# Kernel tuning notes

Measured on AMD Instinct MI355X. Metric: run time of the kernel, lower is better.

## Reference

```python
import jax, jax.numpy as jnp
import numpy as np

B, T = 32, 2048
HID, ACT, SRC, AGE = 512, 64, 2, 16
TRUNK, BINS, PHASES = 256, 20, 7
IN_DIM = HID + ACT + SRC + AGE  # 594


def setup_inputs() -> dict:
    key = jax.random.key(0)
    ks = jax.random.split(key, 16)
    s_in = 1.0 / np.sqrt(IN_DIM)
    s_tr = 1.0 / np.sqrt(TRUNK)
    s_h = 1.0 / np.sqrt(HID)
    return {
        "h_t": jax.random.normal(ks[0], (B, T, HID), jnp.float32),
        "a_t": jax.random.normal(ks[1], (B, T, ACT), jnp.float32),
        "d_t": jax.random.normal(ks[2], (B, T, SRC), jnp.float32),
        "age_embed": jax.random.normal(ks[3], (B, T, AGE), jnp.float32),
        "trunk_w": jax.random.normal(ks[4], (IN_DIM, TRUNK), jnp.float32) * s_in,
        "trunk_b": jax.random.normal(ks[5], (TRUNK,), jnp.float32) * s_in,
        "inst_base_w": jax.random.normal(ks[6], (TRUNK, BINS), jnp.float32) * s_tr,
        "inst_base_b": jax.random.normal(ks[7], (BINS,), jnp.float32) * s_tr,
        "group_base_w": jax.random.normal(ks[8], (TRUNK, BINS), jnp.float32) * s_tr,
        "group_base_b": jax.random.normal(ks[9], (BINS,), jnp.float32) * s_tr,
        "inst_exp_w": jax.random.normal(ks[10], (PHASES, TRUNK, BINS), jnp.float32) * s_tr,
        "inst_exp_b": jax.random.normal(ks[11], (PHASES, BINS), jnp.float32) * s_tr,
        "group_exp_w": jax.random.normal(ks[12], (PHASES, TRUNK, BINS), jnp.float32) * s_tr,
        "group_exp_b": jax.random.normal(ks[13], (PHASES, BINS), jnp.float32) * s_tr,
        "router_w": jax.random.normal(ks[14], (HID, PHASES), jnp.float32) * s_h,
        "router_b": jax.random.normal(ks[15], (PHASES,), jnp.float32) * s_h,
    }


def reference(h_t, a_t, d_t, age_embed,
              trunk_w, trunk_b, inst_base_w, inst_base_b,
              group_base_w, group_base_b, inst_exp_w, inst_exp_b,
              group_exp_w, group_exp_b, router_w, router_b):
    # Shared trunk: Linear(594,256) -> exact GELU
    x = jnp.concatenate([h_t, a_t, d_t, age_embed], axis=-1)  # [B,T,594]
    z = jax.nn.gelu(jnp.einsum('bti,io->bto', x, trunk_w) + trunk_b,
                    approximate=False)  # [B,T,256]

    # Soft phase routing from h_t
    pw = jax.nn.softmax(jnp.einsum('bth,hp->btp', h_t, router_w) + router_b,
                        axis=-1)  # [B,T,7]

    # Base heads
    inst_base = jnp.einsum('btd,dk->btk', z, inst_base_w) + inst_base_b
    group_base = jnp.einsum('btd,dk->btk', z, group_base_w) + group_base_b

    # All 7 experts as one batched GEMM, then weighted reduction over phases
    inst_e = jnp.einsum('btd,pdk->btpk', z, inst_exp_w) + inst_exp_b  # [B,T,7,20]
    group_e = jnp.einsum('btd,pdk->btpk', z, group_exp_w) + group_exp_b
    inst_res = jnp.einsum('btp,btpk->btk', pw, inst_e)
    group_res = jnp.einsum('btp,btpk->btk', pw, group_e)

    return (inst_base + inst_res, group_base + group_res)
```

## Files before the change

### kernel.cpp

```cpp
#include <hip/hip_runtime.h>
#include <math.h>

typedef unsigned int uint;
typedef unsigned short ushort;

using short8 = __attribute__((ext_vector_type(8))) short;
using f32x4  = __attribute__((ext_vector_type(4))) float;

#define BT      65536
#define HID     512
#define IN_DIM  594
#define TRUNK   256
#define BINS    20
#define NCOMBO  320

#define WT_P_SZ (19*16*64*8)
#define RP_SZ   (16*64*8)
#define WA_P_SZ (8*20*64*8)

__device__ inline ushort f2bf(float f) {
    uint u = __float_as_uint(f);
    return (ushort)((u + 0x7fffu + ((u >> 16) & 1u)) >> 16);
}

__global__ __launch_bounds__(64) void pack_all(
    const float* __restrict__ trunk_w, const float* __restrict__ router_w,
    const float* __restrict__ inst_base_w, const float* __restrict__ inst_base_b,
    const float* __restrict__ group_base_w, const float* __restrict__ group_base_b,
    const float* __restrict__ inst_exp_w, const float* __restrict__ inst_exp_b,
    const float* __restrict__ group_exp_w, const float* __restrict__ group_exp_b,
    ushort* __restrict__ WtP, ushort* __restrict__ RP,
    ushort* __restrict__ WaP, float* __restrict__ wbias)
{
    const int b = blockIdx.x, l = threadIdx.x;
    const int lr = l & 15, lg = l >> 4;
    if (b < 304) {
        int kk = b >> 4, n = b & 15;
        int col = n * 16 + lr;
        ushort* dst = WtP + ((size_t)(kk * 16 + n) * 64 + l) * 8;
        #pragma unroll
        for (int j = 0; j < 8; ++j) {
            int k = kk * 32 + lg * 8 + j;
            dst[j] = (k < IN_DIM) ? f2bf(trunk_w[k * TRUNK + col]) : (ushort)0;
        }
    } else if (b < 320) {
        int kk = b - 304;
        ushort* dst = RP + ((size_t)(kk * 64 + l)) * 8;
        #pragma unroll
        for (int j = 0; j < 8; ++j) {
            int k = kk * 32 + lg * 8 + j;
            dst[j] = (lr < 7) ? f2bf(router_w[k * 7 + lr]) : (ushort)0;
        }
    } else if (b < 480) {
        int b2 = b - 320, kk = b2 / 20, n = b2 % 20;
        int combo = n * 16 + lr;
        int h = combo / 160, rem = combo % 160, kb = rem >> 3, p = rem & 7;
        const float* bw = h ? group_base_w : inst_base_w;
        const float* ew = h ? group_exp_w  : inst_exp_w;
        ushort* dst = WaP + ((size_t)(kk * 20 + n) * 64 + l) * 8;
        #pragma unroll
        for (int j = 0; j < 8; ++j) {
            int k = kk * 32 + lg * 8 + j;
            float v = (p == 0) ? bw[k * BINS + kb]
                               : ew[((p - 1) * TRUNK + k) * BINS + kb];
            dst[j] = f2bf(v);
        }
    } else {
        for (int c = l; c < NCOMBO; c += 64) {
            int h = c / 160, rem = c % 160, kb = rem >> 3, p = rem & 7;
            const float* bb = h ? group_base_b : inst_base_b;
            const float* eb = h ? group_exp_b  : inst_exp_b;
            wbias[c] = (p == 0) ? bb[kb] : eb[(p - 1) * BINS + kb];
        }
    }
}

__global__ __launch_bounds__(256, 2) void fused_mfma(
    const float* __restrict__ h_t, const float* __restrict__ a_t,
    const float* __restrict__ d_t, const float* __restrict__ age,
    const float* __restrict__ trunk_b, const float* __restrict__ router_b,
    const ushort* __restrict__ WtP, const ushort* __restrict__ RP,
    const ushort* __restrict__ WaP, const float* __restrict__ wbias,
    float* __restrict__ out)
{
    __shared__ alignas(16) ushort zs[32768];

    const int tid = threadIdx.x;
    const int l = tid & 63, w = tid >> 6;
    const int lr = l & 15, lg = l >> 4;
    const int block0 = blockIdx.x * 128;

    const int srow = tid >> 1;
    const int half = tid & 1;
    const size_t stok = block0 + srow;

    ushort* xs = zs;

    f32x4 acc[8][4];
    f32x4 accr0 = (f32x4){0.f,0.f,0.f,0.f};
    f32x4 accr1 = (f32x4){0.f,0.f,0.f,0.f};
    #pragma unroll
    for (int mm = 0; mm < 8; ++mm)
    #pragma unroll
    for (int nn = 0; nn < 4; ++nn) acc[mm][nn] = (f32x4){0.f,0.f,0.f,0.f};

    auto stage_load = [&](int kk, float4 ld[4]) {
        if (kk < 16) {
            const float4* p = (const float4*)(h_t + stok * HID + kk * 32 + half * 16);
            ld[0]=p[0]; ld[1]=p[1]; ld[2]=p[2]; ld[3]=p[3];
        } else if (kk < 18) {
            const float4* p = (const float4*)(a_t + stok * 64 + (kk - 16) * 32 + half * 16);
            ld[0]=p[0]; ld[1]=p[1]; ld[2]=p[2]; ld[3]=p[3];
        } else {
            float* f = (float*)ld;
            #pragma unroll
            for (int j = 0; j < 16; ++j) {
                int c = 576 + half * 16 + j;
                float v;
                if (c < 578)      v = d_t[stok * 2 + (c - 576)];
                else if (c < 594) v = age[stok * 16 + (c - 578)];
                else              v = 0.f;
                f[j] = v;
            }
        }
    };
    auto stage_write = [&](int buf, float4 ld[4]) {
        const float* f = (const float*)ld;
        short8 v0, v1;
        #pragma unroll
        for (int j = 0; j < 8; ++j) {
            v0[j] = (short)f2bf(f[j]);
            v1[j] = (short)f2bf(f[j + 8]);
        }
        ushort* dst = xs + buf * 4096 + (srow >> 4) * 512 + ((srow & 15) + half * 32) * 8;
        *(short8*)dst = v0;
        *(short8*)(dst + 128) = v1;
    };

    {
        float4 ld[4];
        stage_load(0, ld);
        stage_write(0, ld);
        __syncthreads();
        int cur = 0;
        const int w4 = w * 4;
        #pragma unroll 1
        for (int kk = 0; kk < 19; ++kk) {
            float4 nld[4];
            if (kk < 18) stage_load(kk + 1, nld);

            const ushort* wp = WtP + ((size_t)kk * 16 + w4) * 512;
            short8 bq0 = *(const short8*)(wp + 0 * 512 + l * 8);
            short8 bq1 = *(const short8*)(wp + 1 * 512 + l * 8);
            short8 bq2 = *(const short8*)(wp + 2 * 512 + l * 8);
            short8 bq3 = *(const short8*)(wp + 3 * 512 + l * 8);

            const ushort* xb = xs + cur * 4096;
            short8 a0 = *(const short8*)(xb + 0 * 512 + l * 8);
            short8 a1 = *(const short8*)(xb + 1 * 512 + l * 8);
            short8 a2 = *(const short8*)(xb + 2 * 512 + l * 8);
            short8 a3 = *(const short8*)(xb + 3 * 512 + l * 8);
            short8 a4 = *(const short8*)(xb + 4 * 512 + l * 8);
            short8 a5 = *(const short8*)(xb + 5 * 512 + l * 8);
            short8 a6 = *(const short8*)(xb + 6 * 512 + l * 8);
            short8 a7 = *(const short8*)(xb + 7 * 512 + l * 8);

            if (kk < 16) {
                short8 rb = *(const short8*)(RP + (size_t)kk * 512 + l * 8);
                short8 ar0 = *(const short8*)(xb + (w * 2 + 0) * 512 + l * 8);
                short8 ar1 = *(const short8*)(xb + (w * 2 + 1) * 512 + l * 8);
                accr0 = __builtin_amdgcn_mfma_f32_16x16x32_bf16(ar0, rb, accr0, 0, 0, 0);
                accr1 = __builtin_amdgcn_mfma_f32_16x16x32_bf16(ar1, rb, accr1, 0, 0, 0);
            }

            #define TRUNK_MM(AF) \
                acc[0][0] = __builtin_amdgcn_mfma_f32_16x16x32_bf16(AF, bq0, acc[0][0],0,0,0);
            #undef TRUNK_MM
            #pragma unroll
            for (int nn = 0; nn < 4; ++nn) {
                short8 bq = (nn == 0) ? bq0 : (nn == 1) ? bq1 : (nn == 2) ? bq2 : bq3;
                acc[0][nn] = __builtin_amdgcn_mfma_f32_16x16x32_bf16(a0, bq, acc[0][nn],0,0,0);
                acc[1][nn] = __builtin_amdgcn_mfma_f32_16x16x32_bf16(a1, bq, acc[1][nn],0,0,0);
                acc[2][nn] = __builtin_amdgcn_mfma_f32_16x16x32_bf16(a2, bq, acc[2][nn],0,0,0);
                acc[3][nn] = __builtin_amdgcn_mfma_f32_16x16x32_bf16(a3, bq, acc[3][nn],0,0,0);
                acc[4][nn] = __builtin_amdgcn_mfma_f32_16x16x32_bf16(a4, bq, acc[4][nn],0,0,0);
                acc[5][nn] = __builtin_amdgcn_mfma_f32_16x16x32_bf16(a5, bq, acc[5][nn],0,0,0);
                acc[6][nn] = __builtin_amdgcn_mfma_f32_16x16x32_bf16(a6, bq, acc[6][nn],0,0,0);
                acc[7][nn] = __builtin_amdgcn_mfma_f32_16x16x32_bf16(a7, bq, acc[7][nn],0,0,0);
            }

            if (kk < 18) stage_write(cur ^ 1, nld);
            __syncthreads();
            cur ^= 1;
        }
    }

    float pwv[2][4];
    {
        const float rb_l = (lr < 7) ? router_b[lr] : 0.f;
        #pragma unroll
        for (int m = 0; m < 2; ++m)
        #pragma unroll
        for (int r = 0; r < 4; ++r) {
            float lv = (m == 0) ? accr0[r] : accr1[r];
            float x = (lr < 7) ? (lv + rb_l) : -3.0e38f;
            float mx = x;
            mx = fmaxf(mx, __shfl_xor(mx, 1));
            mx = fmaxf(mx, __shfl_xor(mx, 2));
            mx = fmaxf(mx, __shfl_xor(mx, 4));
            mx = fmaxf(mx, __shfl_xor(mx, 8));
            float e = expf(x - mx);
            float s = e;
            s += __shfl_xor(s, 1);
            s += __shfl_xor(s, 2);
            s += __shfl_xor(s, 4);
            s += __shfl_xor(s, 8);
            pwv[m][r] = e / s;
        }
    }

    {
        char* zb = (char*)zs;
        #pragma unroll
        for (int nn = 0; nn < 4; ++nn) {
            float tb = trunk_b[(w * 4 + nn) * 16 + lr];
            int colbase = (w * 4 + nn) * 16 + lr;
            #pragma unroll
            for (int mm = 0; mm < 8; ++mm)
            #pragma unroll
            for (int r = 0; r < 4; ++r) {
                float v = acc[mm][nn][r] + tb;
                v = 0.5f * v * (1.f + erff(v * 0.70710678118654752f));
                int row  = mm * 16 + lg * 4 + r;
                int slot = (colbase >> 3) ^ (row & 7);
                *(ushort*)(zb + row * 512 + slot * 16 + (colbase & 7) * 2) = f2bf(v);
            }
        }
    }
    __syncthreads();

    const char* zb = (const char*)zs;
    const int p8 = l & 7;
    const int csrc = (l & 48) | (p8 ? (p8 - 1) : 0);
    const int row0 = w * 32 + lr;
    const int row1 = row0 + 16;

    float cw[2][4];
    #pragma unroll
    for (int m = 0; m < 2; ++m)
    #pragma unroll
    for (int r = 0; r < 4; ++r)
        cw[m][r] = __shfl(pwv[m][r], csrc);

    #pragma unroll 1
    for (int hf = 0; hf < 2; ++hf) {
        f32x4 acc2[2][10];
        #pragma unroll
        for (int m = 0; m < 2; ++m)
        #pragma unroll
        for (int n = 0; n < 10; ++n) acc2[m][n] = (f32x4){0.f,0.f,0.f,0.f};
        float wb_[10];
        #pragma unroll
        for (int n = 0; n < 10; ++n) wb_[n] = wbias[(hf * 10 + n) * 16 + lr];

        #pragma unroll
        for (int kk = 0; kk < 8; ++kk) {
            short8 a0 = *(const short8*)(zb + row0 * 512 + (((kk * 4 + lg) ^ (row0 & 7)) << 4));
            short8 a1 = *(const short8*)(zb + row1 * 512 + (((kk * 4 + lg) ^ (row1 & 7)) << 4));
            const ushort* wp = WaP + (size_t)(kk * 20 + hf * 10) * 512;
            #pragma unroll
            for (int n = 0; n < 10; ++n) {
                short8 bq = *(const short8*)(wp + (size_t)n * 512 + l * 8);
                acc2[0][n] = __builtin_amdgcn_mfma_f32_16x16x32_bf16(a0, bq, acc2[0][n],0,0,0);
                acc2[1][n] = __builtin_amdgcn_mfma_f32_16x16x32_bf16(a1, bq, acc2[1][n],0,0,0);
            }
        }

        #pragma unroll
        for (int m = 0; m < 2; ++m)
        #pragma unroll
        for (int n = 0; n < 10; ++n)
        #pragma unroll
        for (int r = 0; r < 4; ++r) {
            float e = acc2[m][n][r] + wb_[n];
            float val = (p8 ? cw[m][r] : 1.0f) * e;
            val += __shfl_xor(val, 1);
            val += __shfl_xor(val, 2);
            val += __shfl_xor(val, 4);
            if (p8 == 0) {
                int combo = (hf * 10 + n) * 16 + lr;
                int h = combo / 160, rem = combo % 160, kb = rem >> 3;
                size_t t = block0 + w * 32 + m * 16 + lg * 4 + r;
                out[(size_t)h * (BT * BINS) + t * BINS + kb] = val;
            }
        }
    }
}

extern "C" void kernel_launch(void* const* d_in, const int* in_sizes, int n_in,
                              void* d_out, int out_size, void* d_ws, size_t ws_size,
                              hipStream_t stream) {
    const float* h_t          = (const float*)d_in[0];
    const float* a_t          = (const float*)d_in[1];
    const float* d_t          = (const float*)d_in[2];
    const float* age_embed    = (const float*)d_in[3];
    const float* trunk_w      = (const float*)d_in[4];
    const float* trunk_b      = (const float*)d_in[5];
    const float* inst_base_w  = (const float*)d_in[6];
    const float* inst_base_b  = (const float*)d_in[7];
    const float* group_base_w = (const float*)d_in[8];
    const float* group_base_b = (const float*)d_in[9];
    const float* inst_exp_w   = (const float*)d_in[10];
    const float* inst_exp_b   = (const float*)d_in[11];
    const float* group_exp_w  = (const float*)d_in[12];
    const float* group_exp_b  = (const float*)d_in[13];
    const float* router_w     = (const float*)d_in[14];
    const float* router_b     = (const float*)d_in[15];

    ushort* WtP   = (ushort*)d_ws;
    ushort* RP    = WtP + WT_P_SZ;
    ushort* WaP   = RP + RP_SZ;
    float*  wbias = (float*)(WaP + WA_P_SZ);

    pack_all<<<481, 64, 0, stream>>>(
        trunk_w, router_w,
        inst_base_w, inst_base_b, group_base_w, group_base_b,
        inst_exp_w, inst_exp_b, group_exp_w, group_exp_b,
        WtP, RP, WaP, wbias);

    fused_mfma<<<BT / 128, 256, 0, stream>>>(
        h_t, a_t, d_t, age_embed, trunk_b, router_b,
        WtP, RP, WaP, wbias, (float*)d_out);
}
```

Before: 92.76 us.

## Halve token tile to 64 rows and repartition head GEMM across waves by columns

Each block now handles 64 tokens instead of 128, which halves shared memory and the trunk accumulator registers, and launch bounds are raised to allow three blocks per CU. The head GEMM is changed from a per-wave row split with two column halves to a per-wave column split (five output tiles per wave) over all 64 rows. The router uses the same A fragments as the trunk instead of loading extra ones. The goal is higher occupancy and twice as many blocks. The cost is that each block reloads the trunk and head weights for fewer tokens.

```diff
diff --git a/kernel.cpp b/kernel.cpp
--- a/kernel.cpp
+++ b/kernel.cpp
@@ -75,7 +75,7 @@
     }
 }
 
-__global__ __launch_bounds__(256, 2) void fused_mfma(
+__global__ __launch_bounds__(256, 3) void fused_mfma(
     const float* __restrict__ h_t, const float* __restrict__ a_t,
     const float* __restrict__ d_t, const float* __restrict__ age,
     const float* __restrict__ trunk_b, const float* __restrict__ router_b,
@@ -83,39 +83,40 @@
     const ushort* __restrict__ WaP, const float* __restrict__ wbias,
     float* __restrict__ out)
 {
-    __shared__ alignas(16) ushort zs[32768];
+    __shared__ alignas(16) ushort zs[16384];
 
     const int tid = threadIdx.x;
     const int l = tid & 63, w = tid >> 6;
     const int lr = l & 15, lg = l >> 4;
-    const int block0 = blockIdx.x * 128;
-
-    const int srow = tid >> 1;
-    const int half = tid & 1;
+    const int block0 = blockIdx.x * 64;
+
+    const int srow = tid >> 2;
+    const int sq   = tid & 3;
     const size_t stok = block0 + srow;
 
     ushort* xs = zs;
 
-    f32x4 acc[8][4];
-    f32x4 accr0 = (f32x4){0.f,0.f,0.f,0.f};
-    f32x4 accr1 = (f32x4){0.f,0.f,0.f,0.f};
+    f32x4 acc[4][4];
+    f32x4 accr[4];
     #pragma unroll
-    for (int mm = 0; mm < 8; ++mm)
-    #pragma unroll
-    for (int nn = 0; nn < 4; ++nn) acc[mm][nn] = (f32x4){0.f,0.f,0.f,0.f};
-
-    auto stage_load = [&](int kk, float4 ld[4]) {
+    for (int mm = 0; mm < 4; ++mm) {
+        accr[mm] = (f32x4){0.f,0.f,0.f,0.f};
+        #pragma unroll
+        for (int nn = 0; nn < 4; ++nn) acc[mm][nn] = (f32x4){0.f,0.f,0.f,0.f};
+    }
+
+    auto stage_load = [&](int kk, float4 ld[2]) {
         if (kk < 16) {
-            const float4* p = (const float4*)(h_t + stok * HID + kk * 32 + half * 16);
-            ld[0]=p[0]; ld[1]=p[1]; ld[2]=p[2]; ld[3]=p[3];
+            const float4* p = (const float4*)(h_t + stok * HID + kk * 32 + sq * 8);
+            ld[0] = p[0]; ld[1] = p[1];
         } else if (kk < 18) {
-            const float4* p = (const float4*)(a_t + stok * 64 + (kk - 16) * 32 + half * 16);
-            ld[0]=p[0]; ld[1]=p[1]; ld[2]=p[2]; ld[3]=p[3];
+            const float4* p = (const float4*)(a_t + stok * 64 + (kk - 16) * 32 + sq * 8);
+            ld[0] = p[0]; ld[1] = p[1];
         } else {
             float* f = (float*)ld;
             #pragma unroll
-            for (int j = 0; j < 16; ++j) {
-                int c = 576 + half * 16 + j;
+            for (int j = 0; j < 8; ++j) {
+                int c = 576 + sq * 8 + j;
                 float v;
                 if (c < 578)      v = d_t[stok * 2 + (c - 576)];
                 else if (c < 594) v = age[stok * 16 + (c - 578)];
@@ -124,69 +125,50 @@
             }
         }
     };
-    auto stage_write = [&](int buf, float4 ld[4]) {
+    auto stage_write = [&](int buf, float4 ld[2]) {
         const float* f = (const float*)ld;
-        short8 v0, v1;
-        #pragma unroll
-        for (int j = 0; j < 8; ++j) {
-            v0[j] = (short)f2bf(f[j]);
-            v1[j] = (short)f2bf(f[j + 8]);
-        }
-        ushort* dst = xs + buf * 4096 + (srow >> 4) * 512 + ((srow & 15) + half * 32) * 8;
-        *(short8*)dst = v0;
-        *(short8*)(dst + 128) = v1;
+        short8 v;
+        #pragma unroll
+        for (int j = 0; j < 8; ++j) v[j] = (short)f2bf(f[j]);
+        *(short8*)(xs + buf * 2048 + ((srow >> 4) * 64 + (srow & 15) + sq * 16) * 8) = v;
     };
 
     {
-        float4 ld[4];
+        float4 ld[2];
         stage_load(0, ld);
         stage_write(0, ld);
         __syncthreads();
         int cur = 0;
-        const int w4 = w * 4;
         #pragma unroll 1
         for (int kk = 0; kk < 19; ++kk) {
-            float4 nld[4];
+            float4 nld[2];
             if (kk < 18) stage_load(kk + 1, nld);
 
-            const ushort* wp = WtP + ((size_t)kk * 16 + w4) * 512;
-            short8 bq0 = *(const short8*)(wp + 0 * 512 + l * 8);
-            short8 bq1 = *(const short8*)(wp + 1 * 512 + l * 8);
-            short8 bq2 = *(const short8*)(wp + 2 * 512 + l * 8);
-            short8 bq3 = *(const short8*)(wp + 3 * 512 + l * 8);
-
-            const ushort* xb = xs + cur * 4096;
-            short8 a0 = *(const short8*)(xb + 0 * 512 + l * 8);
-            short8 a1 = *(const short8*)(xb + 1 * 512 + l * 8);
-            short8 a2 = *(const short8*)(xb + 2 * 512 + l * 8);
-            short8 a3 = *(const short8*)(xb + 3 * 512 + l * 8);
-            short8 a4 = *(const short8*)(xb + 4 * 512 + l * 8);
-            short8 a5 = *(const short8*)(xb + 5 * 512 + l * 8);
-            short8 a6 = *(const short8*)(xb + 6 * 512 + l * 8);
-            short8 a7 = *(const short8*)(xb + 7 * 512 + l * 8);
+            const ushort* xb = xs + cur * 2048;
+            short8 a0 = *(const short8*)(xb + (0 * 64 + l) * 8);
+            short8 a1 = *(const short8*)(xb + (1 * 64 + l) * 8);
+            short8 a2 = *(const short8*)(xb + (2 * 64 + l) * 8);
+            short8 a3 = *(const short8*)(xb + (3 * 64 + l) * 8);
+
+            const ushort* wp = WtP + ((size_t)kk * 16 + w * 4) * 512;
+            short8 bq[4];
+            #pragma unroll
+            for (int nn = 0; nn < 4; ++nn)
+                bq[nn] = *(const short8*)(wp + (size_t)nn * 512 + l * 8);
 
             if (kk < 16) {
                 short8 rb = *(const short8*)(RP + (size_t)kk * 512 + l * 8);
-                short8 ar0 = *(const short8*)(xb + (w * 2 + 0) * 512 + l * 8);
-                short8 ar1 = *(const short8*)(xb + (w * 2 + 1) * 512 + l * 8);
-                accr0 = __builtin_amdgcn_mfma_f32_16x16x32_bf16(ar0, rb, accr0, 0, 0, 0);
-                accr1 = __builtin_amdgcn_mfma_f32_16x16x32_bf16(ar1, rb, accr1, 0, 0, 0);
-            }
-
-            #define TRUNK_MM(AF) \
-                acc[0][0] = __builtin_amdgcn_mfma_f32_16x16x32_bf16(AF, bq0, acc[0][0],0,0,0);
-            #undef TRUNK_MM
+                accr[0] = __builtin_amdgcn_mfma_f32_16x16x32_bf16(a0, rb, accr[0],0,0,0);
+                accr[1] = __builtin_amdgcn_mfma_f32_16x16x32_bf16(a1, rb, accr[1],0,0,0);
+                accr[2] = __builtin_amdgcn_mfma_f32_16x16x32_bf16(a2, rb, accr[2],0,0,0);
+                accr[3] = __builtin_amdgcn_mfma_f32_16x16x32_bf16(a3, rb, accr[3],0,0,0);
+            }
             #pragma unroll
             for (int nn = 0; nn < 4; ++nn) {
-                short8 bq = (nn == 0) ? bq0 : (nn == 1) ? bq1 : (nn == 2) ? bq2 : bq3;
-                acc[0][nn] = __builtin_amdgcn_mfma_f32_16x16x32_bf16(a0, bq, acc[0][nn],0,0,0);
-                acc[1][nn] = __builtin_amdgcn_mfma_f32_16x16x32_bf16(a1, bq, acc[1][nn],0,0,0);
-                acc[2][nn] = __builtin_amdgcn_mfma_f32_16x16x32_bf16(a2, bq, acc[2][nn],0,0,0);
-                acc[3][nn] = __builtin_amdgcn_mfma_f32_16x16x32_bf16(a3, bq, acc[3][nn],0,0,0);
-                acc[4][nn] = __builtin_amdgcn_mfma_f32_16x16x32_bf16(a4, bq, acc[4][nn],0,0,0);
-                acc[5][nn] = __builtin_amdgcn_mfma_f32_16x16x32_bf16(a5, bq, acc[5][nn],0,0,0);
-                acc[6][nn] = __builtin_amdgcn_mfma_f32_16x16x32_bf16(a6, bq, acc[6][nn],0,0,0);
-                acc[7][nn] = __builtin_amdgcn_mfma_f32_16x16x32_bf16(a7, bq, acc[7][nn],0,0,0);
+                acc[0][nn] = __builtin_amdgcn_mfma_f32_16x16x32_bf16(a0, bq[nn], acc[0][nn],0,0,0);
+                acc[1][nn] = __builtin_amdgcn_mfma_f32_16x16x32_bf16(a1, bq[nn], acc[1][nn],0,0,0);
+                acc[2][nn] = __builtin_amdgcn_mfma_f32_16x16x32_bf16(a2, bq[nn], acc[2][nn],0,0,0);
+                acc[3][nn] = __builtin_amdgcn_mfma_f32_16x16x32_bf16(a3, bq[nn], acc[3][nn],0,0,0);
             }
 
             if (kk < 18) stage_write(cur ^ 1, nld);
@@ -195,15 +177,14 @@
         }
     }
 
-    float pwv[2][4];
+    float pwv[4][4];
     {
         const float rb_l = (lr < 7) ? router_b[lr] : 0.f;
         #pragma unroll
-        for (int m = 0; m < 2; ++m)
+        for (int mm = 0; mm < 4; ++mm)
         #pragma unroll
         for (int r = 0; r < 4; ++r) {
-            float lv = (m == 0) ? accr0[r] : accr1[r];
-            float x = (lr < 7) ? (lv + rb_l) : -3.0e38f;
+            float x = (lr < 7) ? (accr[mm][r] + rb_l) : -3.0e38f;
             float mx = x;
             mx = fmaxf(mx, __shfl_xor(mx, 1));
             mx = fmaxf(mx, __shfl_xor(mx, 2));
@@ -215,7 +196,7 @@
             s += __shfl_xor(s, 2);
             s += __shfl_xor(s, 4);
             s += __shfl_xor(s, 8);
-            pwv[m][r] = e / s;
+            pwv[mm][r] = e / s;
         }
     }
 
@@ -223,10 +204,10 @@
         char* zb = (char*)zs;
         #pragma unroll
         for (int nn = 0; nn < 4; ++nn) {
-            float tb = trunk_b[(w * 4 + nn) * 16 + lr];
             int colbase = (w * 4 + nn) * 16 + lr;
-            #pragma unroll
-            for (int mm = 0; mm < 8; ++mm)
+            float tb = trunk_b[colbase];
+            #pragma unroll
+            for (int mm = 0; mm < 4; ++mm)
             #pragma unroll
             for (int r = 0; r < 4; ++r) {
                 float v = acc[mm][nn][r] + tb;
@@ -242,56 +223,58 @@
     const char* zb = (const char*)zs;
     const int p8 = l & 7;
     const int csrc = (l & 48) | (p8 ? (p8 - 1) : 0);
-    const int row0 = w * 32 + lr;
-    const int row1 = row0 + 16;
-
-    float cw[2][4];
+
+    f32x4 acc2[4][5];
     #pragma unroll
-    for (int m = 0; m < 2; ++m)
+    for (int mm = 0; mm < 4; ++mm)
     #pragma unroll
-    for (int r = 0; r < 4; ++r)
-        cw[m][r] = __shfl(pwv[m][r], csrc);
-
-    #pragma unroll 1
-    for (int hf = 0; hf < 2; ++hf) {
-        f32x4 acc2[2][10];
-        #pragma unroll
-        for (int m = 0; m < 2; ++m)
-        #pragma unroll
-        for (int n = 0; n < 10; ++n) acc2[m][n] = (f32x4){0.f,0.f,0.f,0.f};
-        float wb_[10];
-        #pragma unroll
-        for (int n = 0; n < 10; ++n) wb_[n] = wbias[(hf * 10 + n) * 16 + lr];
-
-        #pragma unroll
-        for (int kk = 0; kk < 8; ++kk) {
-            short8 a0 = *(const short8*)(zb + row0 * 512 + (((kk * 4 + lg) ^ (row0 & 7)) << 4));
-            short8 a1 = *(const short8*)(zb + row1 * 512 + (((kk * 4 + lg) ^ (row1 & 7)) << 4));
-            const ushort* wp = WaP + (size_t)(kk * 20 + hf * 10) * 512;
-            #pragma unroll
-            for (int n = 0; n < 10; ++n) {
-                short8 bq = *(const short8*)(wp + (size_t)n * 512 + l * 8);
-                acc2[0][n] = __builtin_amdgcn_mfma_f32_16x16x32_bf16(a0, bq, acc2[0][n],0,0,0);
-                acc2[1][n] = __builtin_amdgcn_mfma_f32_16x16x32_bf16(a1, bq, acc2[1][n],0,0,0);
-            }
-        }
-
-        #pragma unroll
-        for (int m = 0; m < 2; ++m)
-        #pragma unroll
-        for (int n = 0; n < 10; ++n)
-        #pragma unroll
-        for (int r = 0; r < 4; ++r) {
-            float e = acc2[m][n][r] + wb_[n];
-            float val = (p8 ? cw[m][r] : 1.0f) * e;
-            val += __shfl_xor(val, 1);
-            val += __shfl_xor(val, 2);
-            val += __shfl_xor(val, 4);
-            if (p8 == 0) {
-                int combo = (hf * 10 + n) * 16 + lr;
-                int h = combo / 160, rem = combo % 160, kb = rem >> 3;
-                size_t t = block0 + w * 32 + m * 16 + lg * 4 + r;
-                out[(size_t)h * (BT * BINS) + t * BINS + kb] = val;
+    for (int nn = 0; nn < 5; ++nn) acc2[mm][nn] = (f32x4){0.f,0.f,0.f,0.f};
+
+    #pragma unroll
+    for (int kk = 0; kk < 8; ++kk) {
+        short8 a[4];
+        #pragma unroll
+        for (int mm = 0; mm < 4; ++mm) {
+            int row = mm * 16 + lr;
+            a[mm] = *(const short8*)(zb + row * 512 + (((kk * 4 + lg) ^ (row & 7)) << 4));
+        }
+        const ushort* wp = WaP + ((size_t)kk * 20 + w * 5) * 512;
+        #pragma unroll
+        for (int nn = 0; nn < 5; ++nn) {
+            short8 bq = *(const short8*)(wp + (size_t)nn * 512 + l * 8);
+            acc2[0][nn] = __builtin_amdgcn_mfma_f32_16x16x32_bf16(a[0], bq, acc2[0][nn],0,0,0);
+            acc2[1][nn] = __builtin_amdgcn_mfma_f32_16x16x32_bf16(a[1], bq, acc2[1][nn],0,0,0);
+            acc2[2][nn] = __builtin_amdgcn_mfma_f32_16x16x32_bf16(a[2], bq, acc2[2][nn],0,0,0);
+            acc2[3][nn] = __builtin_amdgcn_mfma_f32_16x16x32_bf16(a[3], bq, acc2[3][nn],0,0,0);
+        }
+    }
+
+    {
+        float cw[4][4];
+        #pragma unroll
+        for (int mm = 0; mm < 4; ++mm)
+        #pragma unroll
+        for (int r = 0; r < 4; ++r)
+            cw[mm][r] = __shfl(pwv[mm][r], csrc);
+
+        #pragma unroll
+        for (int nn = 0; nn < 5; ++nn) {
+            int combo = (w * 5 + nn) * 16 + lr;
+            float wb = wbias[combo];
+            #pragma unroll
+            for (int mm = 0; mm < 4; ++mm)
+            #pragma unroll
+            for (int r = 0; r < 4; ++r) {
+                float e = acc2[mm][nn][r] + wb;
+                float val = (p8 ? cw[mm][r] : 1.0f) * e;
+                val += __shfl_xor(val, 1);
+                val += __shfl_xor(val, 2);
+                val += __shfl_xor(val, 4);
+                if (p8 == 0) {
+                    int h = combo / 160, rem = combo % 160, kb = rem >> 3;
+                    size_t t = block0 + mm * 16 + lg * 4 + r;
+                    out[(size_t)h * (BT * BINS) + t * BINS + kb] = val;
+                }
             }
         }
     }
@@ -328,7 +311,7 @@
         inst_exp_w, inst_exp_b, group_exp_w, group_exp_b,
         WtP, RP, WaP, wbias);
 
-    fused_mfma<<<BT / 128, 256, 0, stream>>>(
+    fused_mfma<<<BT / 64, 256, 0, stream>>>(
         h_t, a_t, d_t, age_embed, trunk_b, router_b,
         WtP, RP, WaP, wbias, (float*)d_out);
 }
```

After: 110.9 us. 19.6% more time.

## Triple-buffer trunk input staging with two-deep global prefetch and packed bf16 conversion

Applied to the files above, without the earlier changes.

Changes the trunk GEMM staging from a double-buffered LDS ring with one-step prefetch to a three-slot ring. Global loads are issued two k-chunks ahead, while the bf16 conversion and LDS write trail by one chunk. It also switches the float-to-bf16 conversion to the packed __float22bfloat162_rn intrinsic and replaces __syncthreads with an explicit lgkmcnt wait plus s_barrier. The aim is to hide more global-load latency behind the MFMA work and cut conversion ALU cost, at the price of extra registers for the second in-flight load set, which may lower occupancy.

```diff
diff --git a/kernel.cpp b/kernel.cpp
--- a/kernel.cpp
+++ b/kernel.cpp
@@ -1,4 +1,5 @@
 #include <hip/hip_runtime.h>
+#include <hip/hip_bf16.h>
 #include <math.h>
 
 typedef unsigned int uint;
@@ -21,6 +22,20 @@
 __device__ inline ushort f2bf(float f) {
     uint u = __float_as_uint(f);
     return (ushort)((u + 0x7fffu + ((u >> 16) & 1u)) >> 16);
+}
+
+__device__ inline uint pk2(float lo, float hi) {
+    union { __hip_bfloat162 b; uint u; } cv;
+    cv.b = __float22bfloat162_rn(float2{lo, hi});
+    return cv.u;
+}
+__device__ inline short8 cvt8pk(float4 a, float4 b) {
+    union { uint4 t; short8 s; } cv;
+    cv.t.x = pk2(a.x, a.y);
+    cv.t.y = pk2(a.z, a.w);
+    cv.t.z = pk2(b.x, b.y);
+    cv.t.w = pk2(b.z, b.w);
+    return cv.s;
 }
 
 __global__ __launch_bounds__(64) void pack_all(
@@ -104,15 +119,15 @@
     #pragma unroll
     for (int nn = 0; nn < 4; ++nn) acc[mm][nn] = (f32x4){0.f,0.f,0.f,0.f};
 
-    auto stage_load = [&](int kk, float4 ld[4]) {
+    auto stage_load = [&](int kk, float4* dst) {
         if (kk < 16) {
             const float4* p = (const float4*)(h_t + stok * HID + kk * 32 + half * 16);
-            ld[0]=p[0]; ld[1]=p[1]; ld[2]=p[2]; ld[3]=p[3];
+            dst[0]=p[0]; dst[1]=p[1]; dst[2]=p[2]; dst[3]=p[3];
         } else if (kk < 18) {
             const float4* p = (const float4*)(a_t + stok * 64 + (kk - 16) * 32 + half * 16);
-            ld[0]=p[0]; ld[1]=p[1]; ld[2]=p[2]; ld[3]=p[3];
+            dst[0]=p[0]; dst[1]=p[1]; dst[2]=p[2]; dst[3]=p[3];
         } else {
-            float* f = (float*)ld;
+            float* f = (float*)dst;
             #pragma unroll
             for (int j = 0; j < 16; ++j) {
                 int c = 576 + half * 16 + j;
@@ -124,74 +139,61 @@
             }
         }
     };
-    auto stage_write = [&](int buf, float4 ld[4]) {
-        const float* f = (const float*)ld;
-        short8 v0, v1;
-        #pragma unroll
-        for (int j = 0; j < 8; ++j) {
-            v0[j] = (short)f2bf(f[j]);
-            v1[j] = (short)f2bf(f[j + 8]);
-        }
-        ushort* dst = xs + buf * 4096 + (srow >> 4) * 512 + ((srow & 15) + half * 32) * 8;
+    auto stage_write = [&](int slot, const float4* ld) {
+        short8 v0 = cvt8pk(ld[0], ld[1]);
+        short8 v1 = cvt8pk(ld[2], ld[3]);
+        ushort* dst = xs + slot * 4096
+                      + (srow >> 4) * 512 + ((srow & 15) + half * 32) * 8;
         *(short8*)dst = v0;
         *(short8*)(dst + 128) = v1;
     };
 
+    auto mfma_chunk = [&](const ushort* xb, int kk, bool do_router) {
+        short8 a[8];
+        #pragma unroll
+        for (int mm = 0; mm < 8; ++mm)
+            a[mm] = *(const short8*)(xb + (mm * 64 + l) * 8);
+        if (do_router) {
+            short8 rb  = *(const short8*)(RP + (size_t)kk * 512 + l * 8);
+            short8 ar0 = *(const short8*)(xb + ((2 * w + 0) * 64 + l) * 8);
+            short8 ar1 = *(const short8*)(xb + ((2 * w + 1) * 64 + l) * 8);
+            accr0 = __builtin_amdgcn_mfma_f32_16x16x32_bf16(ar0, rb, accr0, 0, 0, 0);
+            accr1 = __builtin_amdgcn_mfma_f32_16x16x32_bf16(ar1, rb, accr1, 0, 0, 0);
+        }
+        const ushort* wp = WtP + ((size_t)kk * 16 + w * 4) * 512;
+        #pragma unroll
+        for (int nn = 0; nn < 4; ++nn) {
+            short8 bq = *(const short8*)(wp + (size_t)nn * 512 + l * 8);
+            acc[0][nn] = __builtin_amdgcn_mfma_f32_16x16x32_bf16(a[0], bq, acc[0][nn],0,0,0);
+            acc[1][nn] = __builtin_amdgcn_mfma_f32_16x16x32_bf16(a[1], bq, acc[1][nn],0,0,0);
+            acc[2][nn] = __builtin_amdgcn_mfma_f32_16x16x32_bf16(a[2], bq, acc[2][nn],0,0,0);
+            acc[3][nn] = __builtin_amdgcn_mfma_f32_16x16x32_bf16(a[3], bq, acc[3][nn],0,0,0);
+            acc[4][nn] = __builtin_amdgcn_mfma_f32_16x16x32_bf16(a[4], bq, acc[4][nn],0,0,0);
+            acc[5][nn] = __builtin_amdgcn_mfma_f32_16x16x32_bf16(a[5], bq, acc[5][nn],0,0,0);
+            acc[6][nn] = __builtin_amdgcn_mfma_f32_16x16x32_bf16(a[6], bq, acc[6][nn],0,0,0);
+            acc[7][nn] = __builtin_amdgcn_mfma_f32_16x16x32_bf16(a[7], bq, acc[7][nn],0,0,0);
+        }
+    };
+
     {
-        float4 ld[4];
-        stage_load(0, ld);
-        stage_write(0, ld);
-        __syncthreads();
-        int cur = 0;
-        const int w4 = w * 4;
+        float4 rA[4], rB[4];
+        stage_load(0, rA);
+        stage_load(1, rB);
+        stage_write(0, rA);
+        asm volatile("s_waitcnt lgkmcnt(0)" ::: "memory");
+        __builtin_amdgcn_s_barrier();
+
         #pragma unroll 1
         for (int kk = 0; kk < 19; ++kk) {
-            float4 nld[4];
-            if (kk < 18) stage_load(kk + 1, nld);
-
-            const ushort* wp = WtP + ((size_t)kk * 16 + w4) * 512;
-            short8 bq0 = *(const short8*)(wp + 0 * 512 + l * 8);
-            short8 bq1 = *(const short8*)(wp + 1 * 512 + l * 8);
-            short8 bq2 = *(const short8*)(wp + 2 * 512 + l * 8);
-            short8 bq3 = *(const short8*)(wp + 3 * 512 + l * 8);
-
-            const ushort* xb = xs + cur * 4096;
-            short8 a0 = *(const short8*)(xb + 0 * 512 + l * 8);
-            short8 a1 = *(const short8*)(xb + 1 * 512 + l * 8);
-            short8 a2 = *(const short8*)(xb + 2 * 512 + l * 8);
-            short8 a3 = *(const short8*)(xb + 3 * 512 + l * 8);
-            short8 a4 = *(const short8*)(xb + 4 * 512 + l * 8);
-            short8 a5 = *(const short8*)(xb + 5 * 512 + l * 8);
-            short8 a6 = *(const short8*)(xb + 6 * 512 + l * 8);
-            short8 a7 = *(const short8*)(xb + 7 * 512 + l * 8);
-
-            if (kk < 16) {
-                short8 rb = *(const short8*)(RP + (size_t)kk * 512 + l * 8);
-                short8 ar0 = *(const short8*)(xb + (w * 2 + 0) * 512 + l * 8);
-                short8 ar1 = *(const short8*)(xb + (w * 2 + 1) * 512 + l * 8);
-                accr0 = __builtin_amdgcn_mfma_f32_16x16x32_bf16(ar0, rb, accr0, 0, 0, 0);
-                accr1 = __builtin_amdgcn_mfma_f32_16x16x32_bf16(ar1, rb, accr1, 0, 0, 0);
-            }
-
-            #define TRUNK_MM(AF) \
-                acc[0][0] = __builtin_amdgcn_mfma_f32_16x16x32_bf16(AF, bq0, acc[0][0],0,0,0);
-            #undef TRUNK_MM
-            #pragma unroll
-            for (int nn = 0; nn < 4; ++nn) {
-                short8 bq = (nn == 0) ? bq0 : (nn == 1) ? bq1 : (nn == 2) ? bq2 : bq3;
-                acc[0][nn] = __builtin_amdgcn_mfma_f32_16x16x32_bf16(a0, bq, acc[0][nn],0,0,0);
-                acc[1][nn] = __builtin_amdgcn_mfma_f32_16x16x32_bf16(a1, bq, acc[1][nn],0,0,0);
-                acc[2][nn] = __builtin_amdgcn_mfma_f32_16x16x32_bf16(a2, bq, acc[2][nn],0,0,0);
-                acc[3][nn] = __builtin_amdgcn_mfma_f32_16x16x32_bf16(a3, bq, acc[3][nn],0,0,0);
-                acc[4][nn] = __builtin_amdgcn_mfma_f32_16x16x32_bf16(a4, bq, acc[4][nn],0,0,0);
-                acc[5][nn] = __builtin_amdgcn_mfma_f32_16x16x32_bf16(a5, bq, acc[5][nn],0,0,0);
-                acc[6][nn] = __builtin_amdgcn_mfma_f32_16x16x32_bf16(a6, bq, acc[6][nn],0,0,0);
-                acc[7][nn] = __builtin_amdgcn_mfma_f32_16x16x32_bf16(a7, bq, acc[7][nn],0,0,0);
-            }
-
-            if (kk < 18) stage_write(cur ^ 1, nld);
-            __syncthreads();
-            cur ^= 1;
+            float4 rC[4];
+            if (kk + 2 < 19) stage_load(kk + 2, rC);
+            mfma_chunk(xs + (kk % 3) * 4096, kk, kk < 16);
+            if (kk + 1 < 19) stage_write((kk + 1) % 3, rB);
+            asm volatile("s_waitcnt lgkmcnt(0)" ::: "memory");
+            __builtin_amdgcn_s_barrier();
+            if (kk + 2 < 19) {
+                rB[0] = rC[0]; rB[1] = rC[1]; rB[2] = rC[2]; rB[3] = rC[3];
+            }
         }
     }
 
@@ -223,8 +225,8 @@
         char* zb = (char*)zs;
         #pragma unroll
         for (int nn = 0; nn < 4; ++nn) {
-            float tb = trunk_b[(w * 4 + nn) * 16 + lr];
             int colbase = (w * 4 + nn) * 16 + lr;
+            float tb = trunk_b[colbase];
             #pragma unroll
             for (int mm = 0; mm < 8; ++mm)
             #pragma unroll
```

Result: slower. 106.8 us (+15.2%).

## Retile head GEMM as 2x2 wave grid and pack bf16 conversions

Applied to the files above, without the earlier changes.

The second-stage head GEMM changes from each wave owning 32 rows and all 10 column tiles to a 2x2 wave split. Each wave now owns 64 rows and 5 column tiles per half, so every B fragment loaded from global memory feeds 4 MFMAs instead of 2, halving weight traffic per block. Routing weights are exchanged through a small shared-memory table instead of lane shuffles, and the staging conversion to bf16 uses packed float2-to-bfloat162 intrinsics. In exchange there are more LDS A-fragment reads, extra LDS for the routing table, and possibly higher register pressure.

```diff
diff --git a/kernel.cpp b/kernel.cpp
--- a/kernel.cpp
+++ b/kernel.cpp
@@ -1,4 +1,5 @@
 #include <hip/hip_runtime.h>
+#include <hip/hip_bf16.h>
 #include <math.h>
 
 typedef unsigned int uint;
@@ -21,6 +22,20 @@
 __device__ inline ushort f2bf(float f) {
     uint u = __float_as_uint(f);
     return (ushort)((u + 0x7fffu + ((u >> 16) & 1u)) >> 16);
+}
+
+__device__ inline uint pk2(float lo, float hi) {
+    union { __hip_bfloat162 b; uint u; } cv;
+    cv.b = __float22bfloat162_rn(float2{lo, hi});
+    return cv.u;
+}
+__device__ inline short8 cvt8pk(float4 a, float4 b) {
+    union { uint4 t; short8 s; } cv;
+    cv.t.x = pk2(a.x, a.y);
+    cv.t.y = pk2(a.z, a.w);
+    cv.t.z = pk2(b.x, b.y);
+    cv.t.w = pk2(b.z, b.w);
+    return cv.s;
 }
 
 __global__ __launch_bounds__(64) void pack_all(
@@ -84,6 +99,7 @@
     float* __restrict__ out)
 {
     __shared__ alignas(16) ushort zs[32768];
+    __shared__ float pwl[128 * 9];
 
     const int tid = threadIdx.x;
     const int l = tid & 63, w = tid >> 6;
@@ -125,13 +141,8 @@
         }
     };
     auto stage_write = [&](int buf, float4 ld[4]) {
-        const float* f = (const float*)ld;
-        short8 v0, v1;
-        #pragma unroll
-        for (int j = 0; j < 8; ++j) {
-            v0[j] = (short)f2bf(f[j]);
-            v1[j] = (short)f2bf(f[j + 8]);
-        }
+        short8 v0 = cvt8pk(ld[0], ld[1]);
+        short8 v1 = cvt8pk(ld[2], ld[3]);
         ushort* dst = xs + buf * 4096 + (srow >> 4) * 512 + ((srow & 15) + half * 32) * 8;
         *(short8*)dst = v0;
         *(short8*)(dst + 128) = v1;
@@ -173,9 +184,6 @@
                 accr1 = __builtin_amdgcn_mfma_f32_16x16x32_bf16(ar1, rb, accr1, 0, 0, 0);
             }
 
-            #define TRUNK_MM(AF) \
-                acc[0][0] = __builtin_amdgcn_mfma_f32_16x16x32_bf16(AF, bq0, acc[0][0],0,0,0);
-            #undef TRUNK_MM
             #pragma unroll
             for (int nn = 0; nn < 4; ++nn) {
                 short8 bq = (nn == 0) ? bq0 : (nn == 1) ? bq1 : (nn == 2) ? bq2 : bq3;
@@ -195,9 +203,9 @@
         }
     }
 
-    float pwv[2][4];
     {
         const float rb_l = (lr < 7) ? router_b[lr] : 0.f;
+        float pwv[2][4];
         #pragma unroll
         for (int m = 0; m < 2; ++m)
         #pragma unroll
@@ -217,14 +225,21 @@
             s += __shfl_xor(s, 8);
             pwv[m][r] = e / s;
         }
+        if (lr < 7) {
+            #pragma unroll
+            for (int m = 0; m < 2; ++m)
+            #pragma unroll
+            for (int r = 0; r < 4; ++r)
+                pwl[(w * 32 + m * 16 + lg * 4 + r) * 9 + lr] = pwv[m][r];
+        }
     }
 
     {
         char* zb = (char*)zs;
         #pragma unroll
         for (int nn = 0; nn < 4; ++nn) {
-            float tb = trunk_b[(w * 4 + nn) * 16 + lr];
             int colbase = (w * 4 + nn) * 16 + lr;
+            float tb = trunk_b[colbase];
             #pragma unroll
             for (int mm = 0; mm < 8; ++mm)
             #pragma unroll
@@ -240,58 +255,66 @@
     __syncthreads();
 
     const char* zb = (const char*)zs;
+    const int mw = w >> 1;
+    const int nw = w & 1;
     const int p8 = l & 7;
-    const int csrc = (l & 48) | (p8 ? (p8 - 1) : 0);
-    const int row0 = w * 32 + lr;
-    const int row1 = row0 + 16;
-
-    float cw[2][4];
+    const int psel = p8 ? (p8 - 1) : 0;
+
+    float cwv[4][4];
     #pragma unroll
-    for (int m = 0; m < 2; ++m)
+    for (int mm = 0; mm < 4; ++mm)
     #pragma unroll
     for (int r = 0; r < 4; ++r)
-        cw[m][r] = __shfl(pwv[m][r], csrc);
+        cwv[mm][r] = pwl[(mw * 64 + mm * 16 + lg * 4 + r) * 9 + psel];
 
     #pragma unroll 1
     for (int hf = 0; hf < 2; ++hf) {
-        f32x4 acc2[2][10];
-        #pragma unroll
-        for (int m = 0; m < 2; ++m)
-        #pragma unroll
-        for (int n = 0; n < 10; ++n) acc2[m][n] = (f32x4){0.f,0.f,0.f,0.f};
-        float wb_[10];
-        #pragma unroll
-        for (int n = 0; n < 10; ++n) wb_[n] = wbias[(hf * 10 + n) * 16 + lr];
+        const int nbase = nw * 10 + hf * 5;
+        f32x4 acc2[4][5];
+        #pragma unroll
+        for (int mm = 0; mm < 4; ++mm)
+        #pragma unroll
+        for (int n = 0; n < 5; ++n) acc2[mm][n] = (f32x4){0.f,0.f,0.f,0.f};
+        float wb_[5];
+        #pragma unroll
+        for (int n = 0; n < 5; ++n) wb_[n] = wbias[(nbase + n) * 16 + lr];
 
         #pragma unroll
         for (int kk = 0; kk < 8; ++kk) {
-            short8 a0 = *(const short8*)(zb + row0 * 512 + (((kk * 4 + lg) ^ (row0 & 7)) << 4));
-            short8 a1 = *(const short8*)(zb + row1 * 512 + (((kk * 4 + lg) ^ (row1 & 7)) << 4));
-            const ushort* wp = WaP + (size_t)(kk * 20 + hf * 10) * 512;
-            #pragma unroll
-            for (int n = 0; n < 10; ++n) {
+            short8 a[4];
+            #pragma unroll
+            for (int mm = 0; mm < 4; ++mm) {
+                int row = mw * 64 + mm * 16 + lr;
+                a[mm] = *(const short8*)(zb + row * 512 + (((kk * 4 + lg) ^ (row & 7)) << 4));
+            }
+            const ushort* wp = WaP + ((size_t)kk * 20 + nbase) * 512;
+            #pragma unroll
+            for (int n = 0; n < 5; ++n) {
                 short8 bq = *(const short8*)(wp + (size_t)n * 512 + l * 8);
-                acc2[0][n] = __builtin_amdgcn_mfma_f32_16x16x32_bf16(a0, bq, acc2[0][n],0,0,0);
-                acc2[1][n] = __builtin_amdgcn_mfma_f32_16x16x32_bf16(a1, bq, acc2[1][n],0,0,0);
-            }
-        }
-
-        #pragma unroll
-        for (int m = 0; m < 2; ++m)
-        #pragma unroll
-        for (int n = 0; n < 10; ++n)
-        #pragma unroll
-        for (int r = 0; r < 4; ++r) {
-            float e = acc2[m][n][r] + wb_[n];
-            float val = (p8 ? cw[m][r] : 1.0f) * e;
-            val += __shfl_xor(val, 1);
-            val += __shfl_xor(val, 2);
-            val += __shfl_xor(val, 4);
-            if (p8 == 0) {
-                int combo = (hf * 10 + n) * 16 + lr;
-                int h = combo / 160, rem = combo % 160, kb = rem >> 3;
-                size_t t = block0 + w * 32 + m * 16 + lg * 4 + r;
-                out[(size_t)h * (BT * BINS) + t * BINS + kb] = val;
+                acc2[0][n] = __builtin_amdgcn_mfma_f32_16x16x32_bf16(a[0], bq, acc2[0][n],0,0,0);
+                acc2[1][n] = __builtin_amdgcn_mfma_f32_16x16x32_bf16(a[1], bq, acc2[1][n],0,0,0);
+                acc2[2][n] = __builtin_amdgcn_mfma_f32_16x16x32_bf16(a[2], bq, acc2[2][n],0,0,0);
+                acc2[3][n] = __builtin_amdgcn_mfma_f32_16x16x32_bf16(a[3], bq, acc2[3][n],0,0,0);
+            }
+        }
+
+        #pragma unroll
+        for (int n = 0; n < 5; ++n) {
+            int combo = (nbase + n) * 16 + lr;
+            int h = combo / 160, rem = combo % 160, kb = rem >> 3;
+            #pragma unroll
+            for (int mm = 0; mm < 4; ++mm)
+            #pragma unroll
+            for (int r = 0; r < 4; ++r) {
+                float e = acc2[mm][n][r] + wb_[n];
+                float val = (p8 ? cwv[mm][r] : 1.0f) * e;
+                val += __shfl_xor(val, 1);
+                val += __shfl_xor(val, 2);
+                val += __shfl_xor(val, 4);
+                if (p8 == 0) {
+                    size_t t = block0 + mw * 64 + mm * 16 + lg * 4 + r;
+                    out[(size_t)h * (BT * BINS) + t * BINS + kb] = val;
+                }
             }
         }
     }
```

Measured after the change: 103.5 us. 1.12x slower.
